# Kernel tuning notes

Measured on AMD Instinct MI355X. Metric: run time of the kernel, lower is better.

Reference implementation:

```python
import jax, jax.numpy as jnp
import numpy as np

N_PROT = 100000
N_DRUG = 20000
D = 128
E_PPI = 1600000
E_DTI = 800000
LN_EPS = 1e-5


def setup_inputs() -> dict:
    key = jax.random.key(0)
    ks = jax.random.split(key, 11)
    s = 1.0 / np.sqrt(D)
    return {
        "x_prot": jax.random.normal(ks[0], (N_PROT, D), jnp.float32),
        "x_drug": jax.random.normal(ks[1], (N_DRUG, D), jnp.float32),
        "W_gcn": jax.random.normal(ks[2], (D, D), jnp.float32) * s,
        "b_gcn": jnp.zeros((D,), jnp.float32),
        "W_td": jax.random.normal(ks[3], (D, D), jnp.float32) * s,
        "b_td": jnp.zeros((D,), jnp.float32),
        "W_pr": jax.random.normal(ks[4], (D, D), jnp.float32) * s,
        "b_pr": jnp.zeros((D,), jnp.float32),
        "ppi_edge_index": jax.random.randint(ks[5], (2, E_PPI), 0, N_PROT),
        "dti_drug": jax.random.randint(ks[6], (E_DTI,), 0, N_DRUG),
        "dti_prot": jax.random.randint(ks[7], (E_DTI,), 0, N_PROT),
    }


def _gcn_conv(x, W, b, edge_index, num_nodes):
    # PyG GCNConv: add self-loops, symmetric D^-1/2 (A+I) D^-1/2 normalization.
    xw = x @ W  # [N, D_out]
    loops = jnp.arange(num_nodes)
    row = jnp.concatenate([edge_index[0], loops])
    col = jnp.concatenate([edge_index[1], loops])
    deg = jax.ops.segment_sum(jnp.ones_like(col, dtype=xw.dtype), col,
                              num_segments=num_nodes)
    dinv = jnp.where(deg > 0, jax.lax.rsqrt(deg), 0.0)
    norm = dinv[row] * dinv[col]  # [E+N]
    msg = xw[row] * norm[:, None]
    return jax.ops.segment_sum(msg, col, num_segments=num_nodes) + b


def _scatter_mean(vals, idx, num_segments):
    s = jax.ops.segment_sum(vals, idx, num_segments=num_segments)
    cnt = jax.ops.segment_sum(jnp.ones_like(idx, dtype=vals.dtype), idx,
                              num_segments=num_segments)
    return s / jnp.maximum(cnt, 1.0)[:, None]


def _layer_norm(y):
    mu = jnp.mean(y, axis=-1, keepdims=True)
    var = jnp.mean(jnp.square(y - mu), axis=-1, keepdims=True)
    return (y - mu) * jax.lax.rsqrt(var + LN_EPS)


def reference(x_prot, x_drug, W_gcn, b_gcn, W_td, b_td, W_pr, b_pr,
              ppi_edge_index, dti_drug, dti_prot):
    # 'protein' branch of rela_graph_node_update.forward
    x1 = _gcn_conv(x_prot, W_gcn, b_gcn, ppi_edge_index, N_PROT)
    msgs = (x_drug @ W_td + b_td)[dti_drug]  # gather drug messages per dti edge
    x2 = _scatter_mean(msgs, dti_prot, N_PROT)
    x3 = x_prot @ W_pr + b_pr
    return _layer_norm(x1 + x2 + x3 + 1e-6)
```

## Files before the change

kernel.cpp:

```cpp
#include <hip/hip_runtime.h>
#include <hip/hip_bf16.h>

#define D 128
#define NPBK 256
#define NBMAX 512
#define TILE_A 4096
#define SEGMAX 8192

typedef unsigned int uint;
typedef unsigned short ushort;
typedef __attribute__((ext_vector_type(8))) short short8;
typedef __attribute__((ext_vector_type(4))) float f32x4;

static __device__ __forceinline__ float2 bf16x2(uint u) {
  float2 r;
  r.x = __uint_as_float(u << 16);
  r.y = __uint_as_float(u & 0xffff0000u);
  return r;
}

static __device__ __forceinline__ uint pack_bf16x2(float a, float b) {
  __hip_bfloat162 o;
  o.x = __float2bfloat16(a);
  o.y = __float2bfloat16(b);
  return *reinterpret_cast<uint*>(&o);
}

static __device__ __forceinline__ ushort f2bf(float f) {
  __hip_bfloat16 h = __float2bfloat16(f);
  return *reinterpret_cast<ushort*>(&h);
}
static __device__ __forceinline__ float bf2f(ushort u) {
  return __uint_as_float(((uint)u) << 16);
}

static __device__ __forceinline__ void acc8(float* acc, uint4 v) {
  float2 t0 = bf16x2(v.x), t1 = bf16x2(v.y);
  float2 t2 = bf16x2(v.z), t3 = bf16x2(v.w);
  acc[0] += t0.x; acc[1] += t0.y;
  acc[2] += t1.x; acc[3] += t1.y;
  acc[4] += t2.x; acc[5] += t2.y;
  acc[6] += t3.x; acc[7] += t3.y;
}

__global__ void detect_kernel(const uint* __restrict__ x, int n_words,
                              int* __restrict__ flag) {
  __shared__ float smax[256];
  float m = 0.f;
  for (int i = threadIdx.x; i < n_words; i += 256) {
    float2 v = bf16x2(x[i]);
    float a = fabsf(v.x), b = fabsf(v.y);
    if (!(a <= 1e30f)) a = 1e30f;
    if (!(b <= 1e30f)) b = 1e30f;
    m = fmaxf(m, fmaxf(a, b));
  }
  smax[threadIdx.x] = m;
  __syncthreads();
  for (int s = 128; s > 0; s >>= 1) {
    if (threadIdx.x < s)
      smax[threadIdx.x] = fmaxf(smax[threadIdx.x], smax[threadIdx.x + s]);
    __syncthreads();
  }
  if (threadIdx.x == 0) *flag = (smax[0] > 1e6f) ? 1 : 0;
}

__global__ __launch_bounds__(256) void bucket_hist_kernel(
    const int* __restrict__ ppi_col, const int* __restrict__ dti_prot,
    int* __restrict__ gbh, int e_ppi, int e_dti, int n_prot, int nbk) {
  __shared__ int hist[NBMAX];
  const int tid = threadIdx.x;
  for (int b = tid; b < nbk; b += 256) hist[b] = 0;
  __syncthreads();
  const int e_tot = e_ppi + e_dti;
  const int base = blockIdx.x * 8192;
#pragma unroll 4
  for (int j = 0; j < 32; ++j) {
    int i = base + j * 256 + tid;
    if (i < e_tot) {
      int dst = (i < e_ppi) ? ppi_col[i] : dti_prot[i - e_ppi];
      if ((unsigned)dst < (unsigned)n_prot) atomicAdd(&hist[dst >> 8], 1);
    }
  }
  __syncthreads();
  for (int b = tid; b < nbk; b += 256) {
    int h = hist[b];
    if (h) atomicAdd(&gbh[b], h);
  }
}

__global__ __launch_bounds__(NBMAX) void bucket_scan_kernel(
    const int* __restrict__ gbh, int* __restrict__ bbase,
    int* __restrict__ bcur, int nbk) {
  __shared__ int sh[NBMAX];
  const int tid = threadIdx.x;
  int v = (tid < nbk) ? gbh[tid] : 0;
  sh[tid] = v;
  __syncthreads();
  for (int ofs = 1; ofs < NBMAX; ofs <<= 1) {
    int t = (tid >= ofs) ? sh[tid - ofs] : 0;
    __syncthreads();
    sh[tid] += t;
    __syncthreads();
  }
  if (tid < nbk) {
    int e = sh[tid] - v;
    bbase[tid] = e;
    bcur[tid] = e;
    if (tid == nbk - 1) bbase[nbk] = sh[tid];
  }
}

__global__ __launch_bounds__(256) void partition_kernel(
    const int* __restrict__ ppi_row, const int* __restrict__ ppi_col,
    const int* __restrict__ dti_drug, const int* __restrict__ dti_prot,
    int* __restrict__ bcur, uint* __restrict__ P, int e_ppi, int e_dti,
    int n_prot, int nb) {
  __shared__ int hist[NBMAX];
  __shared__ int sh[NBMAX];
  __shared__ int lbase[NBMAX];
  __shared__ int gbase[NBMAX];
  __shared__ int cur[NBMAX];
  __shared__ uint entL[TILE_A];
  __shared__ ushort bktL[TILE_A];
  const int tid = threadIdx.x;
  const int base = blockIdx.x * TILE_A;
  const int e_tot = e_ppi + e_dti;

  for (int b = tid; b < nb; b += 256) hist[b] = 0;
  __syncthreads();

  uint sv[16];
  int dv[16];
#pragma unroll
  for (int j = 0; j < 16; ++j) {
    int i = base + j * 256 + tid;
    int d = -1;
    uint s = 0;
    if (i < e_tot) {
      int src, dst, type;
      if (i < e_ppi) {
        src = ppi_row[i];
        dst = ppi_col[i];
        type = 0;
      } else {
        int k = i - e_ppi;
        src = dti_drug[k];
        dst = dti_prot[k];
        type = 1;
      }
      if ((unsigned)dst < (unsigned)n_prot) {
        d = dst;
        s = (uint)src | ((uint)type << 17);
        atomicAdd(&hist[dst >> 8], 1);
      }
    }
    sv[j] = s;
    dv[j] = d;
  }
  __syncthreads();

  {
    int t2 = tid + 256;
    sh[tid] = (tid < nb) ? hist[tid] : 0;
    sh[t2] = (t2 < nb) ? hist[t2] : 0;
    __syncthreads();
    for (int ofs = 1; ofs < NBMAX; ofs <<= 1) {
      int a0 = (tid >= ofs) ? sh[tid - ofs] : 0;
      int a1 = (t2 >= ofs) ? sh[t2 - ofs] : 0;
      __syncthreads();
      sh[tid] += a0;
      sh[t2] += a1;
      __syncthreads();
    }
  }

  for (int b = tid; b < nb; b += 256) {
    int h = hist[b];
    int lb = sh[b] - h;
    lbase[b] = lb;
    cur[b] = lb;
    gbase[b] = h ? atomicAdd(&bcur[b], h) : 0;
  }
  __syncthreads();

#pragma unroll
  for (int j = 0; j < 16; ++j) {
    if (dv[j] >= 0) {
      int b = dv[j] >> 8;
      int r = atomicAdd(&cur[b], 1);
      entL[r] = sv[j] | ((uint)(dv[j] & (NPBK - 1)) << 18);
      bktL[r] = (ushort)b;
    }
  }
  __syncthreads();

  const int tot = sh[NBMAX - 1];
  for (int u = tid; u < tot; u += 256) {
    int b = bktL[u];
    P[gbase[b] + (u - lbase[b])] = entL[u];
  }
}

__global__ __launch_bounds__(1024) void place_count_kernel(
    const uint* __restrict__ P, const int* __restrict__ bbase,
    uint* __restrict__ csr, int* __restrict__ deg, float* __restrict__ dinv,
    float* __restrict__ invcnt, int* __restrict__ offsets, int n_prot,
    int nbk) {
  __shared__ int degL[NPBK], cntL[NPBK];
  __shared__ int cp[NPBK], cd[NPBK];
  __shared__ int sc[NPBK];
  __shared__ uint srt[SEGMAX];
  const int tid = threadIdx.x;
  const int b = blockIdx.x;
  const int node0 = b * NPBK;
  const int nn = min(NPBK, n_prot - node0);
  const int start = bbase[b], end = bbase[b + 1];
  const int nseg = end - start;

  if (tid < NPBK) {
    degL[tid] = 0;
    cntL[tid] = 0;
  }
  __syncthreads();

  for (int i = start + tid; i < end; i += 1024) {
    uint p = P[i];
    int nl = (int)(p >> 18);
    if ((p >> 17) & 1u)
      atomicAdd(&cntL[nl], 1);
    else
      atomicAdd(&degL[nl], 1);
  }
  __syncthreads();

  int v = 0;
  if (tid < NPBK) {
    v = (tid < nn) ? (degL[tid] + cntL[tid]) : 0;
    sc[tid] = v;
  }
  __syncthreads();
  for (int ofs = 1; ofs < NPBK; ofs <<= 1) {
    int t = 0;
    if (tid < NPBK && tid >= ofs) t = sc[tid - ofs];
    __syncthreads();
    if (tid < NPBK) sc[tid] += t;
    __syncthreads();
  }
  if (tid < nn) {
    int d = degL[tid], c = cntL[tid];
    int lexcl = sc[tid] - v;
    int node = node0 + tid;
    offsets[node] = start + lexcl;
    deg[node] = d;
    dinv[node] = rsqrtf((float)(d + 1));
    invcnt[node] = 1.0f / fmaxf((float)c, 1.0f);
    cp[tid] = lexcl;
    cd[tid] = lexcl + d;
  }
  if (b == nbk - 1 && tid == 0) offsets[n_prot] = end;
  __syncthreads();

  if (nseg <= SEGMAX) {
    for (int i = start + tid; i < end; i += 1024) {
      uint p = P[i];
      int nl = (int)(p >> 18);
      int pos =
          ((p >> 17) & 1u) ? atomicAdd(&cd[nl], 1) : atomicAdd(&cp[nl], 1);
      srt[pos] = p & 0x1ffffu;
    }
    __syncthreads();
    for (int u = tid; u < nseg; u += 1024) csr[start + u] = srt[u];
  } else {
    for (int i = start + tid; i < end; i += 1024) {
      uint p = P[i];
      int nl = (int)(p >> 18);
      int pos =
          ((p >> 17) & 1u) ? atomicAdd(&cd[nl], 1) : atomicAdd(&cp[nl], 1);
      csr[start + pos] = p & 0x1ffffu;
    }
  }
}

__global__ void count_kernel(const int* __restrict__ ppi_col,
                             const int* __restrict__ dti_prot,
                             int* __restrict__ deg, int* __restrict__ cnt,
                             int e_ppi, int e_dti, int n_prot) {
  int i = blockIdx.x * blockDim.x + threadIdx.x;
  if (i < e_ppi) {
    int c = ppi_col[i];
    if ((unsigned)c < (unsigned)n_prot) atomicAdd(&deg[c], 1);
  } else if (i < e_ppi + e_dti) {
    int c = dti_prot[i - e_ppi];
    if ((unsigned)c < (unsigned)n_prot) atomicAdd(&cnt[c], 1);
  }
}

__global__ void block_sum_kernel(const int* __restrict__ deg,
                                 const int* __restrict__ cnt, int n,
                                 float* __restrict__ dinv,
                                 float* __restrict__ invcnt,
                                 int* __restrict__ bsum) {
  __shared__ int sh[256];
  int i = blockIdx.x * 256 + threadIdx.x;
  int t = 0;
  if (i < n) {
    int d = deg[i], c = cnt[i];
    dinv[i] = rsqrtf((float)(d + 1));
    invcnt[i] = 1.0f / fmaxf((float)c, 1.0f);
    t = d + c;
  }
  sh[threadIdx.x] = t;
  __syncthreads();
  for (int s = 128; s > 0; s >>= 1) {
    if (threadIdx.x < s) sh[threadIdx.x] += sh[threadIdx.x + s];
    __syncthreads();
  }
  if (threadIdx.x == 0) bsum[blockIdx.x] = sh[0];
}

__global__ void scan_bsums_kernel(int* __restrict__ bsum, int nb) {
  __shared__ int sh[1024];
  __shared__ int carry;
  int tid = threadIdx.x;
  if (tid == 0) carry = 0;
  __syncthreads();
  for (int base = 0; base < nb; base += 1024) {
    int i = base + tid;
    int v = (i < nb) ? bsum[i] : 0;
    sh[tid] = v;
    __syncthreads();
    for (int ofs = 1; ofs < 1024; ofs <<= 1) {
      int t = (tid >= ofs) ? sh[tid - ofs] : 0;
      __syncthreads();
      sh[tid] += t;
      __syncthreads();
    }
    if (i < nb) bsum[i] = carry + sh[tid] - v;
    int total = sh[1023];
    __syncthreads();
    if (tid == 0) carry += total;
    __syncthreads();
  }
}

__global__ void scan_final_kernel(const int* __restrict__ deg,
                                  const int* __restrict__ cnt,
                                  const int* __restrict__ bbase,
                                  int* __restrict__ offsets, int n) {
  __shared__ int sh[256];
  int tid = threadIdx.x;
  int i = blockIdx.x * 256 + tid;
  int v = (i < n) ? deg[i] + cnt[i] : 0;
  sh[tid] = v;
  __syncthreads();
  for (int ofs = 1; ofs < 256; ofs <<= 1) {
    int t = (tid >= ofs) ? sh[tid - ofs] : 0;
    __syncthreads();
    sh[tid] += t;
    __syncthreads();
  }
  if (i < n) {
    int excl = bbase[blockIdx.x] + sh[tid] - v;
    offsets[i] = excl;
    if (i == n - 1) offsets[n] = excl + v;
  }
}

__global__ void fill_kernel(const int* __restrict__ ppi_row,
                            const int* __restrict__ ppi_col,
                            const int* __restrict__ dti_drug,
                            const int* __restrict__ dti_prot,
                            const int* __restrict__ offsets,
                            const int* __restrict__ deg,
                            int* __restrict__ fposp, int* __restrict__ fposd,
                            uint* __restrict__ csr, int e_ppi, int e_dti,
                            int n_prot) {
  int i = blockIdx.x * blockDim.x + threadIdx.x;
  if (i < e_ppi) {
    int dst = ppi_col[i];
    if ((unsigned)dst >= (unsigned)n_prot) return;
    int pos = offsets[dst] + atomicAdd(&fposp[dst], 1);
    csr[pos] = (uint)ppi_row[i];
  } else if (i < e_ppi + e_dti) {
    int j = i - e_ppi;
    int dst = dti_prot[j];
    if ((unsigned)dst >= (unsigned)n_prot) return;
    int pos = offsets[dst] + deg[dst] + atomicAdd(&fposd[dst], 1);
    csr[pos] = (uint)dti_drug[j];
  }
}

__global__ __launch_bounds__(512) void gemm_prot_mfma(
    const void* __restrict__ X, const void* __restrict__ Wg,
    const void* __restrict__ Wp, const void* __restrict__ bg,
    const void* __restrict__ bp, const float* __restrict__ dinv,
    uint* __restrict__ xw2, void* __restrict__ outx3,
    const int* __restrict__ flag, int M) {
  __shared__ uint4 aF[4][4][2][64];
  __shared__ ushort xwl[64][128];
  const int isf = *flag;
  const int tid = threadIdx.x;
  const int wv = tid >> 6, lane = tid & 63;
  const int cl = lane & 15, kg = lane >> 4;
  const int c = wv * 16 + cl;

  short8 bG[4], bP[4];
#pragma unroll
  for (int kt = 0; kt < 4; ++kt) {
    int k0 = kt * 32 + 8 * kg;
    short8 fg, fp;
    if (isf) {
      const float* WgF = (const float*)Wg;
      const float* WpF = (const float*)Wp;
#pragma unroll
      for (int j = 0; j < 8; ++j) {
        fg[j] = (short)f2bf(WgF[(k0 + j) * D + c]);
        fp[j] = (short)f2bf(WpF[(k0 + j) * D + c]);
      }
    } else {
      const ushort* WgH = (const ushort*)Wg;
      const ushort* WpH = (const ushort*)Wp;
#pragma unroll
      for (int j = 0; j < 8; ++j) {
        fg[j] = (short)WgH[(k0 + j) * D + c];
        fp[j] = (short)WpH[(k0 + j) * D + c];
      }
    }
    bG[kt] = fg;
    bP[kt] = fp;
  }
  float btc;
  {
    float a = isf ? ((const float*)bg)[c] : bf2f(((const ushort*)bg)[c]);
    float b = isf ? ((const float*)bp)[c] : bf2f(((const ushort*)bp)[c]);
    btc = a + b + 1e-6f;
  }

  for (int row0 = blockIdx.x * 64; row0 < M; row0 += gridDim.x * 64) {
    for (int u = tid; u < 1024; u += 512) {
      int row = u >> 4, kc = u & 15;
      int grow = row0 + row;
      uint4 hi = make_uint4(0, 0, 0, 0), lo = make_uint4(0, 0, 0, 0);
      if (isf) {
        if (grow < M) {
          const float4* Xf = (const float4*)X;
          float4 v0 = Xf[(size_t)grow * 32 + kc * 2];
          float4 v1 = Xf[(size_t)grow * 32 + kc * 2 + 1];
          float v[8] = {v0.x, v0.y, v0.z, v0.w, v1.x, v1.y, v1.z, v1.w};
          uint hw[4], lw[4];
#pragma unroll
          for (int j = 0; j < 4; ++j) {
            ushort h0 = f2bf(v[2 * j]), h1 = f2bf(v[2 * j + 1]);
            ushort l0 = f2bf(v[2 * j] - bf2f(h0));
            ushort l1 = f2bf(v[2 * j + 1] - bf2f(h1));
            hw[j] = (uint)h0 | ((uint)h1 << 16);
            lw[j] = (uint)l0 | ((uint)l1 << 16);
          }
          hi = make_uint4(hw[0], hw[1], hw[2], hw[3]);
          lo = make_uint4(lw[0], lw[1], lw[2], lw[3]);
        }
      } else {
        if (grow < M) hi = ((const uint4*)X)[(size_t)grow * 16 + kc];
      }
      int ln = (kc & 3) * 16 + (row & 15);
      int g = row >> 4, kt = kc >> 2;
      aF[g][kt][0][ln] = hi;
      if (isf) aF[g][kt][1][ln] = lo;
    }
    __syncthreads();

#pragma unroll
    for (int g = 0; g < 4; ++g) {
      f32x4 accG = {0.f, 0.f, 0.f, 0.f};
      f32x4 accP = {0.f, 0.f, 0.f, 0.f};
      uint4 aH[4];
#pragma unroll
      for (int kt = 0; kt < 4; ++kt) aH[kt] = aF[g][kt][0][lane];
#pragma unroll
      for (int kt = 0; kt < 4; ++kt) {
        short8 a = __builtin_bit_cast(short8, aH[kt]);
        accG = __builtin_amdgcn_mfma_f32_16x16x32_bf16(a, bG[kt], accG, 0, 0, 0);
        accP = __builtin_amdgcn_mfma_f32_16x16x32_bf16(a, bP[kt], accP, 0, 0, 0);
      }
      if (isf) {
        uint4 aL[4];
#pragma unroll
        for (int kt = 0; kt < 4; ++kt) aL[kt] = aF[g][kt][1][lane];
#pragma unroll
        for (int kt = 0; kt < 4; ++kt) {
          short8 a = __builtin_bit_cast(short8, aL[kt]);
          accG = __builtin_amdgcn_mfma_f32_16x16x32_bf16(a, bG[kt], accG, 0, 0, 0);
          accP = __builtin_amdgcn_mfma_f32_16x16x32_bf16(a, bP[kt], accP, 0, 0, 0);
        }
      }
      int rl0 = g * 16 + kg * 4;
#pragma unroll
      for (int r = 0; r < 4; ++r) {
        int row = row0 + rl0 + r;
        if (row < M) {
          float dn = dinv[row];
          float gv = accG[r], pv = accP[r];
          xwl[rl0 + r][c] = f2bf(gv * dn);
          float ov = fmaf(gv, dn * dn, pv + btc);
          if (isf)
            ((float*)outx3)[(size_t)row * D + c] = ov;
          else
            ((ushort*)outx3)[(size_t)row * D + c] = f2bf(ov);
        }
      }
    }
    __syncthreads();

    int valid = min(64, M - row0);
    const uint4* src = (const uint4*)xwl;
    uint4* dst = (uint4*)xw2 + (size_t)row0 * 16;
    for (int u = tid; u < valid * 16; u += 512) dst[u] = src[u];
  }
}

__global__ __launch_bounds__(512) void gemm_drug_mfma(
    const void* __restrict__ X, const void* __restrict__ W,
    const void* __restrict__ bias, uint* __restrict__ Y2,
    const int* __restrict__ flag, int M) {
  __shared__ uint4 aF[4][4][2][64];
  __shared__ ushort yl[64][128];
  const int isf = *flag;
  const int tid = threadIdx.x;
  const int wv = tid >> 6, lane = tid & 63;
  const int cl = lane & 15, kg = lane >> 4;
  const int c = wv * 16 + cl;

  short8 bT[4];
#pragma unroll
  for (int kt = 0; kt < 4; ++kt) {
    int k0 = kt * 32 + 8 * kg;
    short8 ft;
    if (isf) {
      const float* Wf = (const float*)W;
#pragma unroll
      for (int j = 0; j < 8; ++j) ft[j] = (short)f2bf(Wf[(k0 + j) * D + c]);
    } else {
      const ushort* Wh = (const ushort*)W;
#pragma unroll
      for (int j = 0; j < 8; ++j) ft[j] = (short)Wh[(k0 + j) * D + c];
    }
    bT[kt] = ft;
  }
  float btc = isf ? ((const float*)bias)[c] : bf2f(((const ushort*)bias)[c]);

  for (int row0 = blockIdx.x * 64; row0 < M; row0 += gridDim.x * 64) {
    for (int u = tid; u < 1024; u += 512) {
      int row = u >> 4, kc = u & 15;
      int grow = row0 + row;
      uint4 hi = make_uint4(0, 0, 0, 0), lo = make_uint4(0, 0, 0, 0);
      if (isf) {
        if (grow < M) {
          const float4* Xf = (const float4*)X;
          float4 v0 = Xf[(size_t)grow * 32 + kc * 2];
          float4 v1 = Xf[(size_t)grow * 32 + kc * 2 + 1];
          float v[8] = {v0.x, v0.y, v0.z, v0.w, v1.x, v1.y, v1.z, v1.w};
          uint hw[4], lw[4];
#pragma unroll
          for (int j = 0; j < 4; ++j) {
            ushort h0 = f2bf(v[2 * j]), h1 = f2bf(v[2 * j + 1]);
            ushort l0 = f2bf(v[2 * j] - bf2f(h0));
            ushort l1 = f2bf(v[2 * j + 1] - bf2f(h1));
            hw[j] = (uint)h0 | ((uint)h1 << 16);
            lw[j] = (uint)l0 | ((uint)l1 << 16);
          }
          hi = make_uint4(hw[0], hw[1], hw[2], hw[3]);
          lo = make_uint4(lw[0], lw[1], lw[2], lw[3]);
        }
      } else {
        if (grow < M) hi = ((const uint4*)X)[(size_t)grow * 16 + kc];
      }
      int ln = (kc & 3) * 16 + (row & 15);
      int g = row >> 4, kt = kc >> 2;
      aF[g][kt][0][ln] = hi;
      if (isf) aF[g][kt][1][ln] = lo;
    }
    __syncthreads();

#pragma unroll
    for (int g = 0; g < 4; ++g) {
      f32x4 acc = {0.f, 0.f, 0.f, 0.f};
      uint4 aH[4];
#pragma unroll
      for (int kt = 0; kt < 4; ++kt) aH[kt] = aF[g][kt][0][lane];
#pragma unroll
      for (int kt = 0; kt < 4; ++kt) {
        short8 a = __builtin_bit_cast(short8, aH[kt]);
        acc = __builtin_amdgcn_mfma_f32_16x16x32_bf16(a, bT[kt], acc, 0, 0, 0);
      }
      if (isf) {
        uint4 aL[4];
#pragma unroll
        for (int kt = 0; kt < 4; ++kt) aL[kt] = aF[g][kt][1][lane];
#pragma unroll
        for (int kt = 0; kt < 4; ++kt) {
          short8 a = __builtin_bit_cast(short8, aL[kt]);
          acc = __builtin_amdgcn_mfma_f32_16x16x32_bf16(a, bT[kt], acc, 0, 0, 0);
        }
      }
      int rl0 = g * 16 + kg * 4;
#pragma unroll
      for (int r = 0; r < 4; ++r) {
        int row = row0 + rl0 + r;
        if (row < M) yl[rl0 + r][c] = f2bf(acc[r] + btc);
      }
    }
    __syncthreads();

    int valid = min(64, M - row0);
    const uint4* src = (const uint4*)yl;
    uint4* dst = (uint4*)Y2 + (size_t)row0 * 16;
    for (int u = tid; u < valid * 16; u += 512) dst[u] = src[u];
  }
}

__global__ __launch_bounds__(256) void gather_ln_kernel(
    const uint* __restrict__ xw2, const uint* __restrict__ yd2,
    const float* __restrict__ dinv, const float* __restrict__ invcnt,
    const int* __restrict__ offsets, const int* __restrict__ deg,
    const uint* __restrict__ csr, void* __restrict__ out,
    const int* __restrict__ flag, int n_prot) {
  const int isf = *flag;
  const int node = (blockIdx.x * 256 + threadIdx.x) >> 6;
  const int lane = threadIdx.x & 63;
  const int grp = lane >> 4;
  const int li = lane & 15;
  if (node >= n_prot) return;
  const int s0 = offsets[node];
  const int s1 = offsets[node + 1];
  const int sm = s0 + deg[node];
  const float dn = dinv[node], ic = invcnt[node];

  float aP[8] = {0.f, 0.f, 0.f, 0.f, 0.f, 0.f, 0.f, 0.f};
  float aD[8] = {0.f, 0.f, 0.f, 0.f, 0.f, 0.f, 0.f, 0.f};

  const uint4* X4 = (const uint4*)xw2;
  const uint4* Y4 = (const uint4*)yd2;

#pragma unroll
  for (int part = 0; part < 2; ++part) {
    const uint4* T = part ? Y4 : X4;
    float* acc = part ? aD : aP;
    int a = part ? sm : s0;
    int b = part ? s1 : sm;
    for (int base = a; base < b;) {
      int m = min(64, b - base);
      uint ent = (lane < m) ? csr[base + lane] : 0u;
      int nb4 = m >> 2;
      int t = 0;
      for (; t + 4 <= nb4; t += 4) {
        uint e0 = __shfl(ent, (t + 0) * 4 + grp);
        uint e1 = __shfl(ent, (t + 1) * 4 + grp);
        uint e2 = __shfl(ent, (t + 2) * 4 + grp);
        uint e3 = __shfl(ent, (t + 3) * 4 + grp);
        uint4 w0 = T[(size_t)e0 * 16 + li];
        uint4 w1 = T[(size_t)e1 * 16 + li];
        uint4 w2 = T[(size_t)e2 * 16 + li];
        uint4 w3 = T[(size_t)e3 * 16 + li];
        acc8(acc, w0);
        acc8(acc, w1);
        acc8(acc, w2);
        acc8(acc, w3);
      }
      for (; t < nb4; ++t) {
        uint e = __shfl(ent, t * 4 + grp);
        uint4 w = T[(size_t)e * 16 + li];
        acc8(acc, w);
      }
      int rem = m & 3;
      if (rem) {
        uint e = __shfl(ent, nb4 * 4 + grp);
        if (grp < rem) {
          uint4 w = T[(size_t)e * 16 + li];
          acc8(acc, w);
        }
      }
      base += m;
    }
  }

  float v[8];
#pragma unroll
  for (int i = 0; i < 8; ++i) v[i] = fmaf(dn, aP[i], ic * aD[i]);
#pragma unroll
  for (int i = 0; i < 8; ++i) {
    v[i] += __shfl_xor(v[i], 16);
    v[i] += __shfl_xor(v[i], 32);
  }

  if (isf) {
    const float4* xr = (const float4*)out + (size_t)node * 32 + li * 2;
    float4 x0 = xr[0], x1 = xr[1];
    v[0] += x0.x; v[1] += x0.y; v[2] += x0.z; v[3] += x0.w;
    v[4] += x1.x; v[5] += x1.y; v[6] += x1.z; v[7] += x1.w;
  } else {
    uint4 xr = ((const uint4*)out)[(size_t)node * 16 + li];
    float2 t0 = bf16x2(xr.x), t1 = bf16x2(xr.y);
    float2 t2 = bf16x2(xr.z), t3 = bf16x2(xr.w);
    v[0] += t0.x; v[1] += t0.y; v[2] += t1.x; v[3] += t1.y;
    v[4] += t2.x; v[5] += t2.y; v[6] += t3.x; v[7] += t3.y;
  }

  float s = 0.f, ss = 0.f;
#pragma unroll
  for (int i = 0; i < 8; ++i) {
    s += v[i];
    ss = fmaf(v[i], v[i], ss);
  }
#pragma unroll
  for (int off = 1; off < 16; off <<= 1) {
    s += __shfl_xor(s, off);
    ss += __shfl_xor(ss, off);
  }
  float mu = s * (1.0f / 128.0f);
  float var = ss * (1.0f / 128.0f) - mu * mu;
  float rs = rsqrtf(var + 1e-5f);
#pragma unroll
  for (int i = 0; i < 8; ++i) v[i] = (v[i] - mu) * rs;

  if (isf) {
    if (grp < 2) {
      float4 o = (grp == 0) ? make_float4(v[0], v[1], v[2], v[3])
                            : make_float4(v[4], v[5], v[6], v[7]);
      ((float4*)out)[(size_t)node * 32 + li * 2 + grp] = o;
    }
  } else {
    if (grp == 0) {
      uint4 o;
      o.x = pack_bf16x2(v[0], v[1]);
      o.y = pack_bf16x2(v[2], v[3]);
      o.z = pack_bf16x2(v[4], v[5]);
      o.w = pack_bf16x2(v[6], v[7]);
      ((uint4*)out)[(size_t)node * 16 + li] = o;
    }
  }
}

extern "C" void kernel_launch(void* const* d_in, const int* in_sizes, int n_in,
                              void* d_out, int out_size, void* d_ws,
                              size_t ws_size, hipStream_t stream) {
  const void* x_prot = d_in[0];
  const void* x_drug = d_in[1];
  const void* W_gcn = d_in[2];
  const void* b_gcn = d_in[3];
  const void* W_td = d_in[4];
  const void* b_td = d_in[5];
  const void* W_pr = d_in[6];
  const void* b_pr = d_in[7];
  const int* ppi = (const int*)d_in[8];
  const int* dti_drug = (const int*)d_in[9];
  const int* dti_prot = (const int*)d_in[10];

  int n_prot = in_sizes[0] / D;
  int n_drug = in_sizes[1] / D;
  int e_ppi = in_sizes[8] / 2;
  int e_dti = in_sizes[9];
  int e_tot = e_ppi + e_dti;
  int nb = (n_prot + 255) / 256;
  int nbk = (n_prot + NPBK - 1) / NPBK;

  char* ws = (char*)d_ws;
  size_t off = 0;
  auto alloc = [&](size_t bytes) {
    void* p = ws + off;
    off = (off + bytes + 255) & ~(size_t)255;
    return p;
  };
  int* flag = (int*)alloc(256);
  uint* xw2 = (uint*)alloc((size_t)n_prot * 64 * 4);
  uint* yd2 = (uint*)alloc((size_t)n_drug * 64 * 4);
  int* deg = (int*)alloc((size_t)n_prot * 4);
  int* cnt = (int*)alloc((size_t)n_prot * 4);
  float* dinv = (float*)alloc((size_t)n_prot * 4);
  float* invcnt = (float*)alloc((size_t)n_prot * 4);
  int* offsets = (int*)alloc((size_t)(n_prot + 1) * 4);
  int* fposp = (int*)alloc((size_t)n_prot * 4);
  int* fposd = (int*)alloc((size_t)n_prot * 4);
  int* bsum = (int*)alloc((size_t)nb * 4);
  int* gbh = (int*)alloc((size_t)NBMAX * 4);
  int* bbase = (int*)alloc((size_t)(NBMAX + 1) * 4);
  int* bcur = (int*)alloc((size_t)NBMAX * 4);
  uint* csr = (uint*)alloc((size_t)e_tot * 4);

  if (off > ws_size) return;

  uint* P = xw2;
  bool fast_fill = (n_prot <= (1 << 17)) && (n_drug <= (1 << 17)) &&
                   (nbk <= NBMAX) && ((size_t)e_tot * 4 <= (size_t)n_prot * 256);

  detect_kernel<<<1, 256, 0, stream>>>((const uint*)x_prot, 4096, flag);

  if (fast_fill) {
    hipMemsetAsync(gbh, 0, (size_t)NBMAX * 4, stream);
    bucket_hist_kernel<<<(e_tot + 8191) / 8192, 256, 0, stream>>>(
        ppi + e_ppi, dti_prot, gbh, e_ppi, e_dti, n_prot, nbk);
    bucket_scan_kernel<<<1, NBMAX, 0, stream>>>(gbh, bbase, bcur, nbk);
    partition_kernel<<<(e_tot + TILE_A - 1) / TILE_A, 256, 0, stream>>>(
        ppi, ppi + e_ppi, dti_drug, dti_prot, bcur, P, e_ppi, e_dti, n_prot,
        nbk);
    place_count_kernel<<<nbk, 1024, 0, stream>>>(
        P, bbase, csr, deg, dinv, invcnt, offsets, n_prot, nbk);
  } else {
    hipMemsetAsync(deg, 0, (size_t)n_prot * 4, stream);
    hipMemsetAsync(cnt, 0, (size_t)n_prot * 4, stream);
    hipMemsetAsync(fposp, 0, (size_t)n_prot * 4, stream);
    hipMemsetAsync(fposd, 0, (size_t)n_prot * 4, stream);
    count_kernel<<<(e_tot + 255) / 256, 256, 0, stream>>>(
        ppi + e_ppi, dti_prot, deg, cnt, e_ppi, e_dti, n_prot);
    block_sum_kernel<<<nb, 256, 0, stream>>>(deg, cnt, n_prot, dinv, invcnt,
                                             bsum);
    scan_bsums_kernel<<<1, 1024, 0, stream>>>(bsum, nb);
    scan_final_kernel<<<nb, 256, 0, stream>>>(deg, cnt, bsum, offsets, n_prot);
    fill_kernel<<<(e_tot + 255) / 256, 256, 0, stream>>>(
        ppi, ppi + e_ppi, dti_drug, dti_prot, offsets, deg, fposp, fposd, csr,
        e_ppi, e_dti, n_prot);
  }

  int nbat_p = (n_prot + 63) / 64;
  int grid_p = nbat_p < 512 ? nbat_p : 512;
  gemm_prot_mfma<<<grid_p, 512, 0, stream>>>(x_prot, W_gcn, W_pr, b_gcn, b_pr,
                                             dinv, xw2, d_out, flag, n_prot);
  int nbat_d = (n_drug + 63) / 64;
  int grid_d = nbat_d < 512 ? nbat_d : 512;
  gemm_drug_mfma<<<grid_d, 512, 0, stream>>>(x_drug, W_td, b_td, yd2, flag,
                                             n_drug);

  gather_ln_kernel<<<(n_prot + 3) / 4, 256, 0, stream>>>(
      xw2, yd2, dinv, invcnt, offsets, deg, csr, d_out, flag, n_prot);
}
```

Before: 318.6 us.

## Fold detect and bucket scan into neighbors, fuse prot and drug GEMMs

Cuts the launch count in the fast path. The dtype-detect reduction moves into block 0 of the bucket histogram kernel. The separate bucket scan kernel is removed, so partition and place_count each recompute the global prefix over bucket counts in shared memory. The protein and drug GEMMs are merged into one launch that splits its blocks between the two bodies. The cost is redundant scan work in every partition and place_count block, and one memset that now covers both gbh and gcur, which relies on them being allocated next to each other.

```diff
diff --git a/kernel.cpp b/kernel.cpp
--- a/kernel.cpp
+++ b/kernel.cpp
@@ -66,9 +66,30 @@
 
 __global__ __launch_bounds__(256) void bucket_hist_kernel(
     const int* __restrict__ ppi_col, const int* __restrict__ dti_prot,
-    int* __restrict__ gbh, int e_ppi, int e_dti, int n_prot, int nbk) {
+    int* __restrict__ gbh, const uint* __restrict__ xdet,
+    int* __restrict__ flag, int e_ppi, int e_dti, int n_prot, int nbk) {
   __shared__ int hist[NBMAX];
+  __shared__ float smax[256];
   const int tid = threadIdx.x;
+
+  if (blockIdx.x == 0) {
+    float m = 0.f;
+    for (int i = tid; i < 4096; i += 256) {
+      float2 v = bf16x2(xdet[i]);
+      float a = fabsf(v.x), b = fabsf(v.y);
+      if (!(a <= 1e30f)) a = 1e30f;
+      if (!(b <= 1e30f)) b = 1e30f;
+      m = fmaxf(m, fmaxf(a, b));
+    }
+    smax[tid] = m;
+    __syncthreads();
+    for (int s = 128; s > 0; s >>= 1) {
+      if (tid < s) smax[tid] = fmaxf(smax[tid], smax[tid + s]);
+      __syncthreads();
+    }
+    if (tid == 0) *flag = (smax[0] > 1e6f) ? 1 : 0;
+  }
+
   for (int b = tid; b < nbk; b += 256) hist[b] = 0;
   __syncthreads();
   const int e_tot = e_ppi + e_dti;
@@ -88,45 +109,26 @@
   }
 }
 
-__global__ __launch_bounds__(NBMAX) void bucket_scan_kernel(
-    const int* __restrict__ gbh, int* __restrict__ bbase,
-    int* __restrict__ bcur, int nbk) {
-  __shared__ int sh[NBMAX];
-  const int tid = threadIdx.x;
-  int v = (tid < nbk) ? gbh[tid] : 0;
-  sh[tid] = v;
-  __syncthreads();
-  for (int ofs = 1; ofs < NBMAX; ofs <<= 1) {
-    int t = (tid >= ofs) ? sh[tid - ofs] : 0;
-    __syncthreads();
-    sh[tid] += t;
-    __syncthreads();
-  }
-  if (tid < nbk) {
-    int e = sh[tid] - v;
-    bbase[tid] = e;
-    bcur[tid] = e;
-    if (tid == nbk - 1) bbase[nbk] = sh[tid];
-  }
-}
-
 __global__ __launch_bounds__(256) void partition_kernel(
     const int* __restrict__ ppi_row, const int* __restrict__ ppi_col,
     const int* __restrict__ dti_drug, const int* __restrict__ dti_prot,
-    int* __restrict__ bcur, uint* __restrict__ P, int e_ppi, int e_dti,
-    int n_prot, int nb) {
+    const int* __restrict__ gbh, int* __restrict__ gcur, uint* __restrict__ P,
+    int e_ppi, int e_dti, int n_prot, int nb) {
   __shared__ int hist[NBMAX];
   __shared__ int sh[NBMAX];
   __shared__ int lbase[NBMAX];
   __shared__ int gbase[NBMAX];
   __shared__ int cur[NBMAX];
+  __shared__ int totS;
   __shared__ uint entL[TILE_A];
   __shared__ ushort bktL[TILE_A];
   const int tid = threadIdx.x;
+  const int t2 = tid + 256;
   const int base = blockIdx.x * TILE_A;
   const int e_tot = e_ppi + e_dti;
 
-  for (int b = tid; b < nb; b += 256) hist[b] = 0;
+  hist[tid] = 0;
+  hist[t2] = 0;
   __syncthreads();
 
   uint sv[16];
@@ -159,27 +161,39 @@
   }
   __syncthreads();
 
-  {
-    int t2 = tid + 256;
-    sh[tid] = (tid < nb) ? hist[tid] : 0;
-    sh[t2] = (t2 < nb) ? hist[t2] : 0;
-    __syncthreads();
-    for (int ofs = 1; ofs < NBMAX; ofs <<= 1) {
-      int a0 = (tid >= ofs) ? sh[tid - ofs] : 0;
-      int a1 = (t2 >= ofs) ? sh[t2 - ofs] : 0;
-      __syncthreads();
-      sh[tid] += a0;
-      sh[t2] += a1;
-      __syncthreads();
-    }
-  }
-
-  for (int b = tid; b < nb; b += 256) {
-    int h = hist[b];
-    int lb = sh[b] - h;
+  sh[tid] = hist[tid];
+  sh[t2] = hist[t2];
+  __syncthreads();
+  for (int ofs = 1; ofs < NBMAX; ofs <<= 1) {
+    int a0 = (tid >= ofs) ? sh[tid - ofs] : 0;
+    int a1 = (t2 >= ofs) ? sh[t2 - ofs] : 0;
+    __syncthreads();
+    sh[tid] += a0;
+    sh[t2] += a1;
+    __syncthreads();
+  }
+  for (int b = tid; b < NBMAX; b += 256) {
+    int lb = sh[b] - hist[b];
     lbase[b] = lb;
     cur[b] = lb;
-    gbase[b] = h ? atomicAdd(&bcur[b], h) : 0;
+  }
+  if (tid == 0) totS = sh[NBMAX - 1];
+  __syncthreads();
+
+  sh[tid] = (tid < nb) ? gbh[tid] : 0;
+  sh[t2] = (t2 < nb) ? gbh[t2] : 0;
+  __syncthreads();
+  for (int ofs = 1; ofs < NBMAX; ofs <<= 1) {
+    int a0 = (tid >= ofs) ? sh[tid - ofs] : 0;
+    int a1 = (t2 >= ofs) ? sh[t2 - ofs] : 0;
+    __syncthreads();
+    sh[tid] += a0;
+    sh[t2] += a1;
+    __syncthreads();
+  }
+  for (int b = tid; b < NBMAX; b += 256) {
+    int h = hist[b];
+    gbase[b] = h ? ((b ? sh[b - 1] : 0) + atomicAdd(&gcur[b], h)) : 0;
   }
   __syncthreads();
 
@@ -194,7 +208,7 @@
   }
   __syncthreads();
 
-  const int tot = sh[NBMAX - 1];
+  const int tot = totS;
   for (int u = tid; u < tot; u += 256) {
     int b = bktL[u];
     P[gbase[b] + (u - lbase[b])] = entL[u];
@@ -202,26 +216,41 @@
 }
 
 __global__ __launch_bounds__(1024) void place_count_kernel(
-    const uint* __restrict__ P, const int* __restrict__ bbase,
+    const uint* __restrict__ P, const int* __restrict__ gbh,
     uint* __restrict__ csr, int* __restrict__ deg, float* __restrict__ dinv,
     float* __restrict__ invcnt, int* __restrict__ offsets, int n_prot,
     int nbk) {
   __shared__ int degL[NPBK], cntL[NPBK];
   __shared__ int cp[NPBK], cd[NPBK];
   __shared__ int sc[NPBK];
+  __shared__ int gsh[NBMAX];
+  __shared__ int startS, endS;
   __shared__ uint srt[SEGMAX];
   const int tid = threadIdx.x;
   const int b = blockIdx.x;
   const int node0 = b * NPBK;
   const int nn = min(NPBK, n_prot - node0);
-  const int start = bbase[b], end = bbase[b + 1];
-  const int nseg = end - start;
-
+
+  if (tid < NBMAX) gsh[tid] = (tid < nbk) ? gbh[tid] : 0;
+  __syncthreads();
+  for (int ofs = 1; ofs < NBMAX; ofs <<= 1) {
+    int t = 0;
+    if (tid < NBMAX && tid >= ofs) t = gsh[tid - ofs];
+    __syncthreads();
+    if (tid < NBMAX) gsh[tid] += t;
+    __syncthreads();
+  }
+  if (tid == 0) {
+    startS = b ? gsh[b - 1] : 0;
+    endS = gsh[b];
+  }
   if (tid < NPBK) {
     degL[tid] = 0;
     cntL[tid] = 0;
   }
   __syncthreads();
+  const int start = startS, end = endS;
+  const int nseg = end - start;
 
   for (int i = start + tid; i < end; i += 1024) {
     uint p = P[i];
@@ -390,15 +419,12 @@
   }
 }
 
-__global__ __launch_bounds__(512) void gemm_prot_mfma(
-    const void* __restrict__ X, const void* __restrict__ Wg,
-    const void* __restrict__ Wp, const void* __restrict__ bg,
-    const void* __restrict__ bp, const float* __restrict__ dinv,
-    uint* __restrict__ xw2, void* __restrict__ outx3,
-    const int* __restrict__ flag, int M) {
-  __shared__ uint4 aF[4][4][2][64];
-  __shared__ ushort xwl[64][128];
-  const int isf = *flag;
+static __device__ void gemm_prot_body(
+    uint4 (*aF)[4][2][64], ushort (*xwl)[128], const void* __restrict__ X,
+    const void* __restrict__ Wg, const void* __restrict__ Wp,
+    const void* __restrict__ bg, const void* __restrict__ bp,
+    const float* __restrict__ dinv, uint* __restrict__ xw2,
+    void* __restrict__ outx3, int isf, int M, int bid, int nblk) {
   const int tid = threadIdx.x;
   const int wv = tid >> 6, lane = tid & 63;
   const int cl = lane & 15, kg = lane >> 4;
@@ -436,7 +462,7 @@
     btc = a + b + 1e-6f;
   }
 
-  for (int row0 = blockIdx.x * 64; row0 < M; row0 += gridDim.x * 64) {
+  for (int row0 = bid * 64; row0 < M; row0 += nblk * 64) {
     for (int u = tid; u < 1024; u += 512) {
       int row = u >> 4, kc = u & 15;
       int grow = row0 + row;
@@ -518,13 +544,12 @@
   }
 }
 
-__global__ __launch_bounds__(512) void gemm_drug_mfma(
-    const void* __restrict__ X, const void* __restrict__ W,
-    const void* __restrict__ bias, uint* __restrict__ Y2,
-    const int* __restrict__ flag, int M) {
-  __shared__ uint4 aF[4][4][2][64];
-  __shared__ ushort yl[64][128];
-  const int isf = *flag;
+static __device__ void gemm_drug_body(uint4 (*aF)[4][2][64], ushort (*yl)[128],
+                                      const void* __restrict__ X,
+                                      const void* __restrict__ W,
+                                      const void* __restrict__ bias,
+                                      uint* __restrict__ Y2, int isf, int M,
+                                      int bid, int nblk) {
   const int tid = threadIdx.x;
   const int wv = tid >> 6, lane = tid & 63;
   const int cl = lane & 15, kg = lane >> 4;
@@ -548,7 +573,7 @@
   }
   float btc = isf ? ((const float*)bias)[c] : bf2f(((const ushort*)bias)[c]);
 
-  for (int row0 = blockIdx.x * 64; row0 < M; row0 += gridDim.x * 64) {
+  for (int row0 = bid * 64; row0 < M; row0 += nblk * 64) {
     for (int u = tid; u < 1024; u += 512) {
       int row = u >> 4, kc = u & 15;
       int grow = row0 + row;
@@ -616,6 +641,25 @@
     uint4* dst = (uint4*)Y2 + (size_t)row0 * 16;
     for (int u = tid; u < valid * 16; u += 512) dst[u] = src[u];
   }
+}
+
+__global__ __launch_bounds__(512) void gemm_fused_kernel(
+    const void* __restrict__ Xp, const void* __restrict__ Wg,
+    const void* __restrict__ Wp, const void* __restrict__ bg,
+    const void* __restrict__ bp, const float* __restrict__ dinv,
+    uint* __restrict__ xw2, void* __restrict__ outx3, int Mp, int gp,
+    const void* __restrict__ Xd, const void* __restrict__ Wt,
+    const void* __restrict__ bt, uint* __restrict__ yd2, int Md,
+    const int* __restrict__ flag) {
+  __shared__ uint4 aF[4][4][2][64];
+  __shared__ ushort tb[64][128];
+  const int isf = *flag;
+  if ((int)blockIdx.x < gp)
+    gemm_prot_body(aF, tb, Xp, Wg, Wp, bg, bp, dinv, xw2, outx3, isf, Mp,
+                   blockIdx.x, gp);
+  else
+    gemm_drug_body(aF, tb, Xd, Wt, bt, yd2, isf, Md, blockIdx.x - gp,
+                   gridDim.x - gp);
 }
 
 __global__ __launch_bounds__(256) void gather_ln_kernel(
@@ -782,8 +826,7 @@
   int* fposd = (int*)alloc((size_t)n_prot * 4);
   int* bsum = (int*)alloc((size_t)nb * 4);
   int* gbh = (int*)alloc((size_t)NBMAX * 4);
-  int* bbase = (int*)alloc((size_t)(NBMAX + 1) * 4);
-  int* bcur = (int*)alloc((size_t)NBMAX * 4);
+  int* gcur = (int*)alloc((size_t)NBMAX * 4);
   uint* csr = (uint*)alloc((size_t)e_tot * 4);
 
   if (off > ws_size) return;
@@ -792,19 +835,18 @@
   bool fast_fill = (n_prot <= (1 << 17)) && (n_drug <= (1 << 17)) &&
                    (nbk <= NBMAX) && ((size_t)e_tot * 4 <= (size_t)n_prot * 256);
 
-  detect_kernel<<<1, 256, 0, stream>>>((const uint*)x_prot, 4096, flag);
-
   if (fast_fill) {
-    hipMemsetAsync(gbh, 0, (size_t)NBMAX * 4, stream);
+    hipMemsetAsync(gbh, 0, (size_t)2 * NBMAX * 4, stream);
     bucket_hist_kernel<<<(e_tot + 8191) / 8192, 256, 0, stream>>>(
-        ppi + e_ppi, dti_prot, gbh, e_ppi, e_dti, n_prot, nbk);
-    bucket_scan_kernel<<<1, NBMAX, 0, stream>>>(gbh, bbase, bcur, nbk);
+        ppi + e_ppi, dti_prot, gbh, (const uint*)x_prot, flag, e_ppi, e_dti,
+        n_prot, nbk);
     partition_kernel<<<(e_tot + TILE_A - 1) / TILE_A, 256, 0, stream>>>(
-        ppi, ppi + e_ppi, dti_drug, dti_prot, bcur, P, e_ppi, e_dti, n_prot,
-        nbk);
+        ppi, ppi + e_ppi, dti_drug, dti_prot, gbh, gcur, P, e_ppi, e_dti,
+        n_prot, nbk);
     place_count_kernel<<<nbk, 1024, 0, stream>>>(
-        P, bbase, csr, deg, dinv, invcnt, offsets, n_prot, nbk);
+        P, gbh, csr, deg, dinv, invcnt, offsets, n_prot, nbk);
   } else {
+    detect_kernel<<<1, 256, 0, stream>>>((const uint*)x_prot, 4096, flag);
     hipMemsetAsync(deg, 0, (size_t)n_prot * 4, stream);
     hipMemsetAsync(cnt, 0, (size_t)n_prot * 4, stream);
     hipMemsetAsync(fposp, 0, (size_t)n_prot * 4, stream);
@@ -822,12 +864,11 @@
 
   int nbat_p = (n_prot + 63) / 64;
   int grid_p = nbat_p < 512 ? nbat_p : 512;
-  gemm_prot_mfma<<<grid_p, 512, 0, stream>>>(x_prot, W_gcn, W_pr, b_gcn, b_pr,
-                                             dinv, xw2, d_out, flag, n_prot);
   int nbat_d = (n_drug + 63) / 64;
   int grid_d = nbat_d < 512 ? nbat_d : 512;
-  gemm_drug_mfma<<<grid_d, 512, 0, stream>>>(x_drug, W_td, b_td, yd2, flag,
-                                             n_drug);
+  gemm_fused_kernel<<<grid_p + grid_d, 512, 0, stream>>>(
+      x_prot, W_gcn, W_pr, b_gcn, b_pr, dinv, xw2, d_out, n_prot, grid_p,
+      x_drug, W_td, b_td, yd2, n_drug, flag);
 
   gather_ln_kernel<<<(n_prot + 3) / 4, 256, 0, stream>>>(
       xw2, yd2, dinv, invcnt, offsets, deg, csr, d_out, flag, n_prot);
```

Measured after the change: 308.3 us. -3.2%, faster.
